# Kernel tuning notes

Hardware: AMD Instinct MI355X
Metric: run time of the kernel (lower is better)

The kernel has to match this reference:

```python
import jax, jax.numpy as jnp
import numpy as np

N = 100000
E = 1600000
IN = 64
OUT = 64
K = 4
D = 2
EPS = 1e-15


def setup_inputs() -> dict:
    key = jax.random.key(0)
    ks = jax.random.split(key, 7)
    x = jax.random.normal(ks[0], (N, IN), dtype=jnp.float32)
    edge_index = jax.random.randint(ks[1], (2, E), 0, N, dtype=jnp.int64)
    g = jax.random.normal(ks[2], (IN, K * OUT), dtype=jnp.float32) * (1.0 / np.sqrt(IN))
    mu = jax.random.normal(ks[3], (K, D), dtype=jnp.float32)
    sigma = jax.random.uniform(ks[4], (K, D), dtype=jnp.float32, minval=0.5, maxval=1.5)
    root_w = jax.random.normal(ks[5], (IN, OUT), dtype=jnp.float32) * (1.0 / np.sqrt(IN))
    bias = jnp.zeros((OUT,), dtype=jnp.float32)
    return {"x": x, "edge_index": edge_index, "g": g, "mu": mu,
            "sigma": sigma, "root_w": root_w, "bias": bias}


def reference(x, edge_index, g, mu, sigma, root_w, bias):
    src, dst = edge_index[0], edge_index[1]
    ones = jnp.ones((E,), dtype=x.dtype)
    # in-degree per node, used both for pseudo-coords and for mean aggregation
    deg = jax.ops.segment_sum(ones, dst, num_segments=N)  # [N]
    inv_sqrt_deg = jnp.where(deg > 0, jax.lax.rsqrt(jnp.maximum(deg, 1.0)), 0.0)
    # pseudo-coordinates per edge: [E, 2]
    edge_attr = jnp.stack([inv_sqrt_deg[src], inv_sqrt_deg[dst]], axis=-1)
    # Gaussian mixture kernel weights: [E, K]
    diff = edge_attr[:, None, :] - mu[None, :, :]            # [E,K,D]
    gauss = jnp.exp(jnp.sum(-0.5 * diff * diff / (EPS + sigma[None] ** 2), axis=-1))
    # transform node features once: [N, K, OUT]
    h = (x @ g).reshape(N, K, OUT)
    # gather + per-edge mixture: [E, OUT]
    msg = jnp.einsum('ek,ekm->em', gauss, h[src])
    # mean scatter-aggregate onto destination nodes
    agg = jax.ops.segment_sum(msg, dst, num_segments=N)
    agg = agg / jnp.maximum(deg, 1.0)[:, None]
    return agg + x @ root_w + bias
```

## Files before the change

### kernel.cpp

```cpp
#include <hip/hip_runtime.h>
#include <math.h>

#define N_NODES 100000
#define N_EDGES 1600000
#define IN_F 64
#define OUT_F 64
#define KK 4
#define KY 320
#define EPS 1e-15f
#define NBUCK 391
#define CHUNK 4096
#define BSTRIDE 5120

typedef __attribute__((ext_vector_type(8))) short short8;
typedef __attribute__((ext_vector_type(4))) float float4v;

__device__ int            g_bcur[NBUCK];
__device__ unsigned int   g_binned[NBUCK * BSTRIDE];
__device__ int            g_off[N_NODES + 1];
__device__ float          g_isd[N_NODES];
__device__ float          g_w2[KK * 2];
__device__ unsigned short g_xp[(size_t)N_NODES * IN_F];
__device__ int            g_srcs[N_EDGES];
__device__ unsigned short g_gt[OUT_F * KY];

static __device__ __forceinline__ unsigned short f2bf(float f) {
    unsigned int u = __float_as_uint(f);
    unsigned int r = u + 0x7fffu + ((u >> 16) & 1u);
    return (unsigned short)(r >> 16);
}
static __device__ __forceinline__ float bflo(unsigned int u) { return __uint_as_float(u << 16); }
static __device__ __forceinline__ float bfhi(unsigned int u) { return __uint_as_float(u & 0xffff0000u); }
static __device__ __forceinline__ unsigned int pk(float a, float b) {
    return (unsigned int)f2bf(a) | ((unsigned int)f2bf(b) << 16);
}

__global__ void prep_kernel(const float* __restrict__ x, const float* __restrict__ g,
                            const float* __restrict__ rw, const float* __restrict__ sigma) {
    int t = blockIdx.x * blockDim.x + threadIdx.x;
    if (t < N_NODES * (IN_F / 2)) {
        float a = x[2 * t], b = x[2 * t + 1];
        ((unsigned int*)g_xp)[t] = pk(a, b);
    }
    if (t < NBUCK) g_bcur[t] = 0;
    if (t < KK * 2) {
        float s = sigma[t];
        g_w2[t] = -0.5f / (EPS + s * s);
    }
    if (t < OUT_F * KY) {
        int o = t / KY, kk = t % KY;
        float v;
        if (kk < 256) {
            int k = kk >> 6, i = kk & 63;
            v = g[i * 256 + k * 64 + o];
        } else {
            v = rw[(kk - 256) * 64 + o];
        }
        g_gt[o * KY + kk] = f2bf(v);
    }
}

__global__ __launch_bounds__(256, 4) void binA1_kernel(const int* __restrict__ src,
                                                       const int* __restrict__ dst) {
    __shared__ unsigned int   s_ent[CHUNK];
    __shared__ unsigned short s_bkt[CHUNK];
    __shared__ int s_hist[NBUCK];
    __shared__ int s_off[448];
    __shared__ int s_gbase[NBUCK];
    __shared__ int s_cur[NBUCK];
    int t = threadIdx.x;
    int e0 = blockIdx.x * CHUNK;
    int nvalid = N_EDGES - e0; if (nvalid > CHUNK) nvalid = CHUNK;

    int myb[16];
    unsigned int mye[16];
#pragma unroll
    for (int r = 0; r < 16; ++r) {
        int e = e0 + r * 256 + t;
        if (e < N_EDGES) {
            int s = src[e], d = dst[e];
            myb[r] = d >> 8;
            mye[r] = ((unsigned int)s << 8) | (unsigned int)(d & 255);
        } else myb[r] = -1;
    }
    for (int i = t; i < NBUCK; i += 256) { s_hist[i] = 0; s_cur[i] = 0; }
    __syncthreads();
#pragma unroll
    for (int r = 0; r < 16; ++r)
        if (myb[r] >= 0) atomicAdd(&s_hist[myb[r]], 1);
    __syncthreads();
    if (t < 64) {
        int carry = 0;
        for (int seg = 0; seg < 7; ++seg) {
            int idx = seg * 64 + t;
            int v = (idx < NBUCK) ? s_hist[idx] : 0;
            int orig = v;
#pragma unroll
            for (int d = 1; d < 64; d <<= 1) {
                int u = __shfl_up(v, d);
                if (t >= d) v += u;
            }
            s_off[idx] = carry + v - orig;
            carry += __shfl(v, 63);
        }
    }
    __syncthreads();
    for (int i = t; i < NBUCK; i += 256) {
        int c = s_hist[i];
        s_gbase[i] = (c > 0) ? atomicAdd(&g_bcur[i], c) : 0;
    }
    __syncthreads();
#pragma unroll
    for (int r = 0; r < 16; ++r) {
        int b = myb[r];
        if (b >= 0) {
            int slot = s_off[b] + atomicAdd(&s_cur[b], 1);
            s_ent[slot] = mye[r];
            s_bkt[slot] = (unsigned short)b;
        }
    }
    __syncthreads();
    for (int slot = t; slot < nvalid; slot += 256) {
        int b = s_bkt[slot];
        int pos = b * BSTRIDE + s_gbase[b] + (slot - s_off[b]);
        g_binned[pos] = s_ent[slot];
    }
}

__global__ __launch_bounds__(256, 4) void binA2_kernel() {
    __shared__ int s_hist[256], s_off[256], s_cur[256];
    __shared__ int s_red[4];
    int b = blockIdx.x;
    int t = threadIdx.x;
    int cnt = g_bcur[b];
    int part = 0;
    for (int i = t; i < b; i += 256) part += g_bcur[i];
#pragma unroll
    for (int d = 32; d >= 1; d >>= 1) part += __shfl_down(part, d);
    if ((t & 63) == 0) s_red[t >> 6] = part;
    s_hist[t] = 0; s_cur[t] = 0;
    __syncthreads();
    int gbase = s_red[0] + s_red[1] + s_red[2] + s_red[3];
    int n0 = b * 256;
    const unsigned int* ent = g_binned + (size_t)b * BSTRIDE;
    for (int i = t; i < cnt; i += 256) atomicAdd(&s_hist[ent[i] & 255u], 1);
    __syncthreads();
    if (t < 64) {
        int carry = 0;
        for (int seg = 0; seg < 4; ++seg) {
            int idx = seg * 64 + t;
            int v = s_hist[idx];
            int orig = v;
#pragma unroll
            for (int d = 1; d < 64; d <<= 1) {
                int u = __shfl_up(v, d);
                if (t >= d) v += u;
            }
            s_off[idx] = carry + v - orig;
            carry += __shfl(v, 63);
        }
    }
    __syncthreads();
    int n = n0 + t;
    if (n < N_NODES) {
        g_off[n] = gbase + s_off[t];
        int c = s_hist[t];
        g_isd[n] = (c > 0) ? rsqrtf((float)c) : 0.0f;
    }
    if (b == NBUCK - 1 && t == 0) g_off[N_NODES] = N_EDGES;
    __syncthreads();
    for (int i = t; i < cnt; i += 256) {
        unsigned int e = ent[i];
        int dl = e & 255u;
        int pos = gbase + s_off[dl] + atomicAdd(&s_cur[dl], 1);
        g_srcs[pos] = (int)(e >> 8);
    }
}

__global__ __launch_bounds__(256, 4) void fused_kernel(const float* __restrict__ mu,
                                                       const float* __restrict__ bias,
                                                       float* __restrict__ out) {
    __shared__ unsigned short yt[32][328];
    int t = threadIdx.x;
    int wv = t >> 6, L = t & 63;
    int grp = L >> 3, c = L & 7;
    int n0 = blockIdx.x * 32;
    int n = n0 + wv * 8 + grp;

    int off = g_off[n], end = g_off[n + 1];
    int cdeg = end - off;
    float mu0[KK], w20[KK], t1[KK];
    {
        float a1 = (cdeg > 0) ? rsqrtf((float)cdeg) : 0.0f;
#pragma unroll
        for (int k = 0; k < KK; ++k) {
            mu0[k] = mu[k * 2 + 0];
            w20[k] = g_w2[k * 2 + 0];
            float d1 = a1 - mu[k * 2 + 1];
            t1[k] = g_w2[k * 2 + 1] * d1 * d1;
        }
    }

    float y[KK][8];
#pragma unroll
    for (int k = 0; k < KK; ++k)
#pragma unroll
        for (int i = 0; i < 8; ++i) y[k][i] = 0.0f;

    int j = off;
    for (; j + 3 < end; j += 4) {
        int s0 = g_srcs[j], s1 = g_srcs[j + 1], s2 = g_srcs[j + 2], s3 = g_srcs[j + 3];
        float a0 = g_isd[s0], a1 = g_isd[s1], a2 = g_isd[s2], a3 = g_isd[s3];
        uint4 x0 = *(const uint4*)(g_xp + (size_t)s0 * IN_F + c * 8);
        uint4 x1 = *(const uint4*)(g_xp + (size_t)s1 * IN_F + c * 8);
        uint4 x2 = *(const uint4*)(g_xp + (size_t)s2 * IN_F + c * 8);
        uint4 x3 = *(const uint4*)(g_xp + (size_t)s3 * IN_F + c * 8);
        float w0[KK], w1[KK], w2v[KK], w3[KK];
#pragma unroll
        for (int k = 0; k < KK; ++k) {
            float d0;
            d0 = a0 - mu0[k]; w0[k]  = __expf(w20[k] * d0 * d0 + t1[k]);
            d0 = a1 - mu0[k]; w1[k]  = __expf(w20[k] * d0 * d0 + t1[k]);
            d0 = a2 - mu0[k]; w2v[k] = __expf(w20[k] * d0 * d0 + t1[k]);
            d0 = a3 - mu0[k]; w3[k]  = __expf(w20[k] * d0 * d0 + t1[k]);
        }
        float f0[8] = {bflo(x0.x), bfhi(x0.x), bflo(x0.y), bfhi(x0.y),
                       bflo(x0.z), bfhi(x0.z), bflo(x0.w), bfhi(x0.w)};
        float f1[8] = {bflo(x1.x), bfhi(x1.x), bflo(x1.y), bfhi(x1.y),
                       bflo(x1.z), bfhi(x1.z), bflo(x1.w), bfhi(x1.w)};
        float f2[8] = {bflo(x2.x), bfhi(x2.x), bflo(x2.y), bfhi(x2.y),
                       bflo(x2.z), bfhi(x2.z), bflo(x2.w), bfhi(x2.w)};
        float f3[8] = {bflo(x3.x), bfhi(x3.x), bflo(x3.y), bfhi(x3.y),
                       bflo(x3.z), bfhi(x3.z), bflo(x3.w), bfhi(x3.w)};
#pragma unroll
        for (int k = 0; k < KK; ++k)
#pragma unroll
            for (int i = 0; i < 8; ++i)
                y[k][i] += w0[k] * f0[i] + w1[k] * f1[i] + w2v[k] * f2[i] + w3[k] * f3[i];
    }
    for (; j < end; ++j) {
        int s0 = g_srcs[j];
        float a0 = g_isd[s0];
        uint4 x0 = *(const uint4*)(g_xp + (size_t)s0 * IN_F + c * 8);
        float w0[KK];
#pragma unroll
        for (int k = 0; k < KK; ++k) {
            float d0 = a0 - mu0[k];
            w0[k] = __expf(w20[k] * d0 * d0 + t1[k]);
        }
        float f0[8] = {bflo(x0.x), bfhi(x0.x), bflo(x0.y), bfhi(x0.y),
                       bflo(x0.z), bfhi(x0.z), bflo(x0.w), bfhi(x0.w)};
#pragma unroll
        for (int k = 0; k < KK; ++k)
#pragma unroll
            for (int i = 0; i < 8; ++i) y[k][i] += w0[k] * f0[i];
    }

    float inv = 1.0f / ((cdeg > 0) ? (float)cdeg : 1.0f);
    int row = wv * 8 + grp;
#pragma unroll
    for (int k = 0; k < KK; ++k) {
        uint4 v;
        v.x = pk(y[k][0] * inv, y[k][1] * inv);
        v.y = pk(y[k][2] * inv, y[k][3] * inv);
        v.z = pk(y[k][4] * inv, y[k][5] * inv);
        v.w = pk(y[k][6] * inv, y[k][7] * inv);
        *(uint4*)&yt[row][k * 64 + c * 8] = v;
    }
    *(uint4*)&yt[row][256 + c * 8] = *(const uint4*)(g_xp + (size_t)n * IN_F + c * 8);
    __syncthreads();

    int m = L & 15, q = L >> 4;
    int o = wv * 16 + m;
    float bv = bias[o];
#pragma unroll
    for (int T = 0; T < 2; ++T) {
        float4v acc = {0.f, 0.f, 0.f, 0.f};
#pragma unroll
        for (int s = 0; s < 10; ++s) {
            short8 a = *(const short8*)&yt[T * 16 + m][s * 32 + q * 8];
            short8 b = *(const short8*)&g_gt[(size_t)o * KY + s * 32 + q * 8];
            acc = __builtin_amdgcn_mfma_f32_16x16x32_bf16(a, b, acc, 0, 0, 0);
        }
#pragma unroll
        for (int r = 0; r < 4; ++r) {
            int node = n0 + T * 16 + q * 4 + r;
            out[(size_t)node * OUT_F + o] = acc[r] + bv;
        }
    }
}

extern "C" void kernel_launch(void* const* d_in, const int* in_sizes, int n_in,
                              void* d_out, int out_size, void* d_ws, size_t ws_size,
                              hipStream_t stream) {
    const float* x     = (const float*)d_in[0];
    const int*   ei    = (const int*)d_in[1];
    const float* g     = (const float*)d_in[2];
    const float* mu    = (const float*)d_in[3];
    const float* sigma = (const float*)d_in[4];
    const float* rw    = (const float*)d_in[5];
    const float* bias  = (const float*)d_in[6];
    float* out = (float*)d_out;

    const int* src = ei;
    const int* dst = ei + N_EDGES;

    prep_kernel<<<(N_NODES * 32 + 255) / 256, 256, 0, stream>>>(x, g, rw, sigma);
    binA1_kernel<<<(N_EDGES + CHUNK - 1) / CHUNK, 256, 0, stream>>>(src, dst);
    binA2_kernel<<<NBUCK, 256, 0, stream>>>();
    fused_kernel<<<N_NODES / 32, 256, 0, stream>>>(mu, bias, out);
}
```

Before: 203.7 us.

## Halve bucket size in binning and software-pipeline edge index loads in aggregation

The binning pass now uses 128-node buckets (782 buckets, 2048-edge chunks), so there are twice as many blocks in both binning kernels. The prefix scan in binA1 is rewritten as a 4-wave scan to cover the larger bucket count. The fused aggregation loop now prefetches the next four source indices and their degree scales while the current feature gathers are processed, shortening the dependent load chain. The costs are more global atomics on bucket counters and extra registers for the prefetched values.

```diff
diff --git a/kernel.cpp b/kernel.cpp
--- a/kernel.cpp
+++ b/kernel.cpp
@@ -8,9 +8,10 @@
 #define KK 4
 #define KY 320
 #define EPS 1e-15f
-#define NBUCK 391
-#define CHUNK 4096
-#define BSTRIDE 5120
+#define NBUCK 782
+#define BNODES 128
+#define CHUNK 2048
+#define BSTRIDE 2560
 
 typedef __attribute__((ext_vector_type(8))) short short8;
 typedef __attribute__((ext_vector_type(4))) float float4v;
@@ -65,44 +66,54 @@
     __shared__ unsigned int   s_ent[CHUNK];
     __shared__ unsigned short s_bkt[CHUNK];
     __shared__ int s_hist[NBUCK];
-    __shared__ int s_off[448];
+    __shared__ int s_off[NBUCK];
     __shared__ int s_gbase[NBUCK];
     __shared__ int s_cur[NBUCK];
+    __shared__ int s_wsum[4];
     int t = threadIdx.x;
+    int lane = t & 63, wv = t >> 6;
     int e0 = blockIdx.x * CHUNK;
     int nvalid = N_EDGES - e0; if (nvalid > CHUNK) nvalid = CHUNK;
 
-    int myb[16];
-    unsigned int mye[16];
-#pragma unroll
-    for (int r = 0; r < 16; ++r) {
+    int myb[8];
+    unsigned int mye[8];
+#pragma unroll
+    for (int r = 0; r < 8; ++r) {
         int e = e0 + r * 256 + t;
         if (e < N_EDGES) {
             int s = src[e], d = dst[e];
-            myb[r] = d >> 8;
-            mye[r] = ((unsigned int)s << 8) | (unsigned int)(d & 255);
+            myb[r] = d >> 7;
+            mye[r] = ((unsigned int)s << 7) | (unsigned int)(d & 127);
         } else myb[r] = -1;
     }
     for (int i = t; i < NBUCK; i += 256) { s_hist[i] = 0; s_cur[i] = 0; }
     __syncthreads();
 #pragma unroll
-    for (int r = 0; r < 16; ++r)
+    for (int r = 0; r < 8; ++r)
         if (myb[r] >= 0) atomicAdd(&s_hist[myb[r]], 1);
     __syncthreads();
-    if (t < 64) {
+    {
+        int b0 = t * 4;
+        int v0 = (b0 + 0 < NBUCK) ? s_hist[b0 + 0] : 0;
+        int v1 = (b0 + 1 < NBUCK) ? s_hist[b0 + 1] : 0;
+        int v2 = (b0 + 2 < NBUCK) ? s_hist[b0 + 2] : 0;
+        int v3 = (b0 + 3 < NBUCK) ? s_hist[b0 + 3] : 0;
+        int p = v0 + v1 + v2 + v3;
+        int sc = p;
+#pragma unroll
+        for (int d = 1; d < 64; d <<= 1) {
+            int u = __shfl_up(sc, d);
+            if (lane >= d) sc += u;
+        }
+        if (lane == 63) s_wsum[wv] = sc;
+        __syncthreads();
         int carry = 0;
-        for (int seg = 0; seg < 7; ++seg) {
-            int idx = seg * 64 + t;
-            int v = (idx < NBUCK) ? s_hist[idx] : 0;
-            int orig = v;
-#pragma unroll
-            for (int d = 1; d < 64; d <<= 1) {
-                int u = __shfl_up(v, d);
-                if (t >= d) v += u;
-            }
-            s_off[idx] = carry + v - orig;
-            carry += __shfl(v, 63);
-        }
+        for (int w = 0; w < wv; ++w) carry += s_wsum[w];
+        int excl = carry + sc - p;
+        if (b0 + 0 < NBUCK) s_off[b0 + 0] = excl;
+        if (b0 + 1 < NBUCK) s_off[b0 + 1] = excl + v0;
+        if (b0 + 2 < NBUCK) s_off[b0 + 2] = excl + v0 + v1;
+        if (b0 + 3 < NBUCK) s_off[b0 + 3] = excl + v0 + v1 + v2;
     }
     __syncthreads();
     for (int i = t; i < NBUCK; i += 256) {
@@ -111,7 +122,7 @@
     }
     __syncthreads();
 #pragma unroll
-    for (int r = 0; r < 16; ++r) {
+    for (int r = 0; r < 8; ++r) {
         int b = myb[r];
         if (b >= 0) {
             int slot = s_off[b] + atomicAdd(&s_cur[b], 1);
@@ -128,52 +139,53 @@
 }
 
 __global__ __launch_bounds__(256, 4) void binA2_kernel() {
-    __shared__ int s_hist[256], s_off[256], s_cur[256];
+    __shared__ int s_hist[BNODES], s_off[BNODES], s_cur[BNODES];
     __shared__ int s_red[4];
+    __shared__ int s_w2sum[2];
     int b = blockIdx.x;
     int t = threadIdx.x;
+    int lane = t & 63;
     int cnt = g_bcur[b];
     int part = 0;
     for (int i = t; i < b; i += 256) part += g_bcur[i];
 #pragma unroll
     for (int d = 32; d >= 1; d >>= 1) part += __shfl_down(part, d);
-    if ((t & 63) == 0) s_red[t >> 6] = part;
-    s_hist[t] = 0; s_cur[t] = 0;
+    if (lane == 0) s_red[t >> 6] = part;
+    for (int i = t; i < BNODES; i += 256) { s_hist[i] = 0; s_cur[i] = 0; }
     __syncthreads();
     int gbase = s_red[0] + s_red[1] + s_red[2] + s_red[3];
-    int n0 = b * 256;
+    int n0 = b * BNODES;
     const unsigned int* ent = g_binned + (size_t)b * BSTRIDE;
-    for (int i = t; i < cnt; i += 256) atomicAdd(&s_hist[ent[i] & 255u], 1);
-    __syncthreads();
-    if (t < 64) {
-        int carry = 0;
-        for (int seg = 0; seg < 4; ++seg) {
-            int idx = seg * 64 + t;
-            int v = s_hist[idx];
-            int orig = v;
-#pragma unroll
-            for (int d = 1; d < 64; d <<= 1) {
-                int u = __shfl_up(v, d);
-                if (t >= d) v += u;
-            }
-            s_off[idx] = carry + v - orig;
-            carry += __shfl(v, 63);
-        }
-    }
-    __syncthreads();
-    int n = n0 + t;
-    if (n < N_NODES) {
-        g_off[n] = gbase + s_off[t];
-        int c = s_hist[t];
-        g_isd[n] = (c > 0) ? rsqrtf((float)c) : 0.0f;
+    for (int i = t; i < cnt; i += 256) atomicAdd(&s_hist[ent[i] & 127u], 1);
+    __syncthreads();
+    int sc = 0, v = 0;
+    if (t < BNODES) {
+        v = s_hist[t];
+        sc = v;
+#pragma unroll
+        for (int d = 1; d < 64; d <<= 1) {
+            int u = __shfl_up(sc, d);
+            if (lane >= d) sc += u;
+        }
+        if (lane == 63) s_w2sum[t >> 6] = sc;
+    }
+    __syncthreads();
+    if (t < BNODES) {
+        int carry = (t >= 64) ? s_w2sum[0] : 0;
+        s_off[t] = carry + sc - v;
+        int n = n0 + t;
+        if (n < N_NODES) {
+            g_off[n] = gbase + s_off[t];
+            g_isd[n] = (v > 0) ? rsqrtf((float)v) : 0.0f;
+        }
     }
     if (b == NBUCK - 1 && t == 0) g_off[N_NODES] = N_EDGES;
     __syncthreads();
     for (int i = t; i < cnt; i += 256) {
         unsigned int e = ent[i];
-        int dl = e & 255u;
+        int dl = e & 127u;
         int pos = gbase + s_off[dl] + atomicAdd(&s_cur[dl], 1);
-        g_srcs[pos] = (int)(e >> 8);
+        g_srcs[pos] = (int)(e >> 7);
     }
 }
 
@@ -208,13 +220,25 @@
         for (int i = 0; i < 8; ++i) y[k][i] = 0.0f;
 
     int j = off;
-    for (; j + 3 < end; j += 4) {
-        int s0 = g_srcs[j], s1 = g_srcs[j + 1], s2 = g_srcs[j + 2], s3 = g_srcs[j + 3];
-        float a0 = g_isd[s0], a1 = g_isd[s1], a2 = g_isd[s2], a3 = g_isd[s3];
+    int s0 = 0, s1 = 0, s2 = 0, s3 = 0;
+    float a0 = 0.f, a1 = 0.f, a2 = 0.f, a3 = 0.f;
+    if (j + 3 < end) {
+        s0 = g_srcs[j]; s1 = g_srcs[j + 1]; s2 = g_srcs[j + 2]; s3 = g_srcs[j + 3];
+        a0 = g_isd[s0]; a1 = g_isd[s1]; a2 = g_isd[s2]; a3 = g_isd[s3];
+    }
+    for (; j + 3 < end; ) {
         uint4 x0 = *(const uint4*)(g_xp + (size_t)s0 * IN_F + c * 8);
         uint4 x1 = *(const uint4*)(g_xp + (size_t)s1 * IN_F + c * 8);
         uint4 x2 = *(const uint4*)(g_xp + (size_t)s2 * IN_F + c * 8);
         uint4 x3 = *(const uint4*)(g_xp + (size_t)s3 * IN_F + c * 8);
+        int jn = j + 4;
+        int ns0 = 0, ns1 = 0, ns2 = 0, ns3 = 0;
+        float na0 = 0.f, na1 = 0.f, na2 = 0.f, na3 = 0.f;
+        bool more = (jn + 3 < end);
+        if (more) {
+            ns0 = g_srcs[jn]; ns1 = g_srcs[jn + 1]; ns2 = g_srcs[jn + 2]; ns3 = g_srcs[jn + 3];
+            na0 = g_isd[ns0]; na1 = g_isd[ns1]; na2 = g_isd[ns2]; na3 = g_isd[ns3];
+        }
         float w0[KK], w1[KK], w2v[KK], w3[KK];
 #pragma unroll
         for (int k = 0; k < KK; ++k) {
@@ -237,15 +261,18 @@
 #pragma unroll
             for (int i = 0; i < 8; ++i)
                 y[k][i] += w0[k] * f0[i] + w1[k] * f1[i] + w2v[k] * f2[i] + w3[k] * f3[i];
+        s0 = ns0; s1 = ns1; s2 = ns2; s3 = ns3;
+        a0 = na0; a1 = na1; a2 = na2; a3 = na3;
+        j = jn;
     }
     for (; j < end; ++j) {
-        int s0 = g_srcs[j];
-        float a0 = g_isd[s0];
-        uint4 x0 = *(const uint4*)(g_xp + (size_t)s0 * IN_F + c * 8);
+        int ss = g_srcs[j];
+        float aa = g_isd[ss];
+        uint4 x0 = *(const uint4*)(g_xp + (size_t)ss * IN_F + c * 8);
         float w0[KK];
 #pragma unroll
         for (int k = 0; k < KK; ++k) {
-            float d0 = a0 - mu0[k];
+            float d0 = aa - mu0[k];
             w0[k] = __expf(w20[k] * d0 * d0 + t1[k]);
         }
         float f0[8] = {bflo(x0.x), bfhi(x0.x), bflo(x0.y), bfhi(x0.y),
```

Measured after the change: 213.9 us. 5.0% more time.
